# Kernel tuning notes

Hardware: AMD Instinct MI355X
Metric: run time of the kernel (lower is better)

## Reference

```python
import jax, jax.numpy as jnp
import numpy as np

EPS = 0.1
MAX_ITER = 100
THRESH = 0.1


def setup_inputs() -> dict:
    key = jax.random.key(0)
    k1, k2, k3, k4 = jax.random.split(key, 4)
    N, P1, P2, D = 4, 1024, 1024, 16
    x = jax.random.normal(k1, (N, P1, D), dtype=jnp.float32)
    y = jax.random.normal(k2, (N, P2, D), dtype=jnp.float32)
    wx = jax.random.uniform(k3, (N, P1), dtype=jnp.float32)
    wy = jax.random.uniform(k4, (N, P2), dtype=jnp.float32)
    # normalize to probability weights (typical usage for empirical measures)
    wx = wx / jnp.sum(wx, axis=-1, keepdims=True)
    wy = wy / jnp.sum(wy, axis=-1, keepdims=True)
    return {"x": x, "y": y, "wx": wx, "wy": wy}


def _cost_matrix(x, y):
    # |x_i - y_j|^1 summed over feature dim -> [N, P1, P2]
    return jnp.sum(jnp.abs(x[:, :, None, :] - y[:, None, :, :]), axis=-1)


def reference(x, y, wx, wy):
    C = _cost_matrix(x, y)                     # [N, P1, P2]
    mu, nu = wx, wy                            # [N, P1], [N, P2]
    log_mu = jnp.log(mu + 1e-8)
    log_nu = jnp.log(nu + 1e-8)

    def M(u, v):
        # (-C_ij + u_i + v_j) / eps
        return (-C + u[:, :, None] + v[:, None, :]) / EPS

    def step(carry, _):
        u, v, done = carry
        u_new = EPS * (log_mu - jax.nn.logsumexp(M(u, v), axis=-1)) + u
        v_new = EPS * (log_nu - jax.nn.logsumexp(M(u_new, v), axis=-2)) + v
        err = jnp.mean(jnp.sum(jnp.abs(u_new - u), axis=-1))
        # emulate torch's early break: freeze u,v once converged
        u_out = jnp.where(done, u, u_new)
        v_out = jnp.where(done, v, v_new)
        done = done | (err < THRESH)
        return (u_out, v_out, done), None

    u0 = jnp.zeros_like(mu)
    v0 = jnp.zeros_like(nu)
    (u, v, _), _ = jax.lax.scan(step, (u0, v0, jnp.array(False)), None, length=MAX_ITER)

    pi = jnp.exp(M(u, v))                      # transport plan [N, P1, P2]
    cost = jnp.sum(pi * C, axis=(-2, -1))      # [N]  (reduction='none')
    return cost, pi, C
```

## Files before the change

### kernel.cpp

```cpp
#include <hip/hip_runtime.h>

static constexpr int   NB      = 4;
static constexpr int   PP      = 1024;
static constexpr int   DD      = 16;
static constexpr float EPSV    = 0.1f;
static constexpr float KE      = 14.42695041f;
static constexpr float KL      = 0.0693147181f;
static constexpr int   MAXIT   = 100;
static constexpr float THRESHV = 0.1f;

static constexpr int NBLK = 256;
static constexpr int NTHR = 512;

__device__ __forceinline__ float fexp2(float v) { return __builtin_amdgcn_exp2f(v); }
__device__ __forceinline__ float flog2(float v) { return __builtin_amdgcn_logf(v); }

static constexpr size_t WS_BYTES = (4096 + 16) * 4;

static constexpr int VSNAP_OFF = 131072;
static constexpr int ERR_OFF   = 262144;

__device__ __forceinline__ float aload(const float* p) {
    return __hip_atomic_load(p, __ATOMIC_RELAXED, __HIP_MEMORY_SCOPE_AGENT);
}
__device__ __forceinline__ void astore(float* p, float v) {
    __hip_atomic_store(p, v, __ATOMIC_RELAXED, __HIP_MEMORY_SCOPE_AGENT);
}
__device__ __forceinline__ unsigned aloadu(const unsigned* p) {
    return __hip_atomic_load(p, __ATOMIC_RELAXED, __HIP_MEMORY_SCOPE_AGENT);
}
__device__ __forceinline__ void astoreu(unsigned* p, unsigned v) {
    __hip_atomic_store(p, v, __ATOMIC_RELAXED, __HIP_MEMORY_SCOPE_AGENT);
}
__device__ __forceinline__ float2 aload2(const float* p) {
    unsigned long long v = __hip_atomic_load((const unsigned long long*)p,
                                             __ATOMIC_RELAXED, __HIP_MEMORY_SCOPE_AGENT);
    union { unsigned long long u; float f[2]; } c; c.u = v;
    return make_float2(c.f[0], c.f[1]);
}
__device__ __forceinline__ void astore2(float* p, float a, float b) {
    union { unsigned long long u; float f[2]; } c; c.f[0] = a; c.f[1] = b;
    __hip_atomic_store((unsigned long long*)p, c.u,
                       __ATOMIC_RELAXED, __HIP_MEMORY_SCOPE_AGENT);
}

__device__ __forceinline__ void gbar_group(unsigned* ws32, int n, int g, unsigned gen) {
    __syncthreads();
    if (threadIdx.x < 64) {
        if (threadIdx.x == 0) astoreu(ws32 + (n * 64 + g) * 16, gen);
        const unsigned* sp = ws32 + (n * 64 + threadIdx.x) * 16;
        while (__ballot(aloadu(sp) >= gen) != ~0ull)
            __builtin_amdgcn_s_sleep(1);
    }
    __syncthreads();
}
__device__ __forceinline__ void gbar_all(unsigned* ws32, int b, unsigned gen) {
    __syncthreads();
    if (threadIdx.x < 64) {
        if (threadIdx.x == 0) astoreu(ws32 + b * 16, gen);
        for (;;) {
            bool ok = true;
            #pragma unroll
            for (int q = 0; q < 4; ++q)
                ok &= (aloadu(ws32 + (q * 64 + threadIdx.x) * 16) >= gen);
            if (__ballot(ok) == ~0ull) break;
            __builtin_amdgcn_s_sleep(1);
        }
    }
    __syncthreads();
}

__global__ __launch_bounds__(NTHR, 2)
void sinkhorn_kernel(const float* __restrict__ x, const float* __restrict__ y,
                     const float* __restrict__ wx, const float* __restrict__ wy,
                     float* __restrict__ out, float* __restrict__ ws)
{
    __shared__ float rt[16 * PP];
    __shared__ float sbuf[PP];
    __shared__ float cred[8];
    __shared__ int   Ts;

    unsigned* ws32 = (unsigned*)ws;
    unsigned* Tslot = ws32 + 4096;

    float* out_cost = out;
    float* out_pi   = out + NB;
    float* out_C    = out + NB + (size_t)NB * PP * PP;

    const int b   = blockIdx.x;
    const int n   = b >> 6;
    const int g   = b & 63;
    const int i0  = g * 16;
    const int w   = threadIdx.x >> 6;
    const int l   = threadIdx.x & 63;
    const int tid = threadIdx.x;

    float* sc  = out_C + (size_t)n * PP * PP;
    float* esc = sc + ERR_OFF;

    float4 xr[2][4];
    #pragma unroll
    for (int rr = 0; rr < 2; ++rr) {
        const float4* xp = (const float4*)(x + ((size_t)n * PP + (i0 + 2 * w + rr)) * DD);
        #pragma unroll
        for (int q = 0; q < 4; ++q) xr[rr][q] = xp[q];
    }
    #pragma unroll 4
    for (int k = 0; k < 16; ++k) {
        int j = l + 64 * k;
        const float4* yp = (const float4*)(y + ((size_t)n * PP + j) * DD);
        float4 y0 = yp[0], y1 = yp[1], y2 = yp[2], y3 = yp[3];
        #pragma unroll
        for (int rr = 0; rr < 2; ++rr) {
            float c = fabsf(xr[rr][0].x - y0.x) + fabsf(xr[rr][0].y - y0.y)
                    + fabsf(xr[rr][0].z - y0.z) + fabsf(xr[rr][0].w - y0.w)
                    + fabsf(xr[rr][1].x - y1.x) + fabsf(xr[rr][1].y - y1.y)
                    + fabsf(xr[rr][1].z - y1.z) + fabsf(xr[rr][1].w - y1.w)
                    + fabsf(xr[rr][2].x - y2.x) + fabsf(xr[rr][2].y - y2.y)
                    + fabsf(xr[rr][2].z - y2.z) + fabsf(xr[rr][2].w - y2.w)
                    + fabsf(xr[rr][3].x - y3.x) + fabsf(xr[rr][3].y - y3.y)
                    + fabsf(xr[rr][3].z - y3.z) + fabsf(xr[rr][3].w - y3.w);
            rt[(2 * w + rr) * PP + j] = c;
        }
    }

    float4 yc[2][4];
    #pragma unroll
    for (int c = 0; c < 2; ++c) {
        const float4* yp = (const float4*)(y + ((size_t)n * PP + (i0 + 2 * w + c)) * DD);
        #pragma unroll
        for (int q = 0; q < 4; ++q) yc[c][q] = yp[q];
    }
    float2 c2[16];
    #pragma unroll 4
    for (int k = 0; k < 16; ++k) {
        const float4* xp = (const float4*)(x + ((size_t)n * PP + (l + 64 * k)) * DD);
        float4 x0 = xp[0], x1 = xp[1], x2 = xp[2], x3 = xp[3];
        float cc[2];
        #pragma unroll
        for (int c = 0; c < 2; ++c) {
            cc[c] = fabsf(x0.x - yc[c][0].x) + fabsf(x0.y - yc[c][0].y)
                  + fabsf(x0.z - yc[c][0].z) + fabsf(x0.w - yc[c][0].w)
                  + fabsf(x1.x - yc[c][1].x) + fabsf(x1.y - yc[c][1].y)
                  + fabsf(x1.z - yc[c][1].z) + fabsf(x1.w - yc[c][1].w)
                  + fabsf(x2.x - yc[c][2].x) + fabsf(x2.y - yc[c][2].y)
                  + fabsf(x2.z - yc[c][2].z) + fabsf(x2.w - yc[c][2].w)
                  + fabsf(x3.x - yc[c][3].x) + fabsf(x3.y - yc[c][3].y)
                  + fabsf(x3.z - yc[c][3].z) + fabsf(x3.w - yc[c][3].w);
        }
        c2[k] = make_float2(cc[0], cc[1]);
    }

    float u_loc[2], lmu[2], lnu[2];
    #pragma unroll
    for (int rr = 0; rr < 2; ++rr) {
        u_loc[rr] = 0.f;
        lmu[rr] = __logf(wx[n * PP + i0 + 2 * w + rr] + 1e-8f);
        lnu[rr] = __logf(wy[n * PP + i0 + 2 * w + rr] + 1e-8f);
    }

    #pragma unroll 1
    for (int t = 0; t < MAXIT; ++t) {
        if (t == 0) {
            sbuf[2 * tid] = 0.f; sbuf[2 * tid + 1] = 0.f;
        } else {
            float2 vp = aload2(sc + VSNAP_OFF + (size_t)(t - 1) * PP + 2 * tid);
            sbuf[2 * tid] = vp.x; sbuf[2 * tid + 1] = vp.y;
        }
        __syncthreads();

        float unew[2], werr;
        {
            float4 tt[2][4];
            float m0 = -3.4e38f, m1 = -3.4e38f;
            #pragma unroll
            for (int k = 0; k < 4; ++k) {
                int j = 256 * k + 4 * l;
                float4 v4 = *(const float4*)&sbuf[j];
                float4 ca = *(const float4*)&rt[(2 * w) * PP + j];
                float4 cb = *(const float4*)&rt[(2 * w + 1) * PP + j];
                tt[0][k] = make_float4(v4.x - ca.x, v4.y - ca.y, v4.z - ca.z, v4.w - ca.w);
                tt[1][k] = make_float4(v4.x - cb.x, v4.y - cb.y, v4.z - cb.z, v4.w - cb.w);
                m0 = fmaxf(m0, fmaxf(fmaxf(tt[0][k].x, tt[0][k].y), fmaxf(tt[0][k].z, tt[0][k].w)));
                m1 = fmaxf(m1, fmaxf(fmaxf(tt[1][k].x, tt[1][k].y), fmaxf(tt[1][k].z, tt[1][k].w)));
            }
            #pragma unroll
            for (int off = 32; off >= 1; off >>= 1) {
                m0 = fmaxf(m0, __shfl_xor(m0, off));
                m1 = fmaxf(m1, __shfl_xor(m1, off));
            }
            float s0 = 0.f, s1 = 0.f;
            #pragma unroll
            for (int k = 0; k < 4; ++k) {
                s0 += fexp2((tt[0][k].x - m0) * KE) + fexp2((tt[0][k].y - m0) * KE)
                    + fexp2((tt[0][k].z - m0) * KE) + fexp2((tt[0][k].w - m0) * KE);
                s1 += fexp2((tt[1][k].x - m1) * KE) + fexp2((tt[1][k].y - m1) * KE)
                    + fexp2((tt[1][k].z - m1) * KE) + fexp2((tt[1][k].w - m1) * KE);
            }
            #pragma unroll
            for (int off = 32; off >= 1; off >>= 1) {
                s0 += __shfl_xor(s0, off);
                s1 += __shfl_xor(s1, off);
            }
            unew[0] = EPSV * lmu[0] - (m0 + KL * flog2(s0));
            unew[1] = EPSV * lmu[1] - (m1 + KL * flog2(s1));
            werr = fabsf(unew[0] - u_loc[0]) + fabsf(unew[1] - u_loc[1]);
            u_loc[0] = unew[0]; u_loc[1] = unew[1];
            if (l == 0) {
                astore2(sc + (size_t)t * PP + i0 + 2 * w, unew[0], unew[1]);
                cred[w] = werr;
            }
        }

        __syncthreads();
        if (tid < 64) {
            if (tid == 0) {
                float es = cred[0] + cred[1] + cred[2] + cred[3]
                         + cred[4] + cred[5] + cred[6] + cred[7];
                astore(esc + t * 64 + g, es);
                astoreu(ws32 + (n * 64 + g) * 16, (unsigned)(2 * t + 1));
            }
            const unsigned* sp = ws32 + (n * 64 + tid) * 16;
            while (__ballot(aloadu(sp) >= (unsigned)(2 * t + 1)) != ~0ull)
                __builtin_amdgcn_s_sleep(1);
        }
        __syncthreads();

        {
            float2 up = aload2(sc + (size_t)t * PP + 2 * tid);
            sbuf[2 * tid] = up.x; sbuf[2 * tid + 1] = up.y;
        }
        __syncthreads();

        float vnew[2];
        {
            float tt0[16], tt1[16], m0 = -3.4e38f, m1 = -3.4e38f;
            #pragma unroll
            for (int k = 0; k < 16; ++k) {
                float uu = sbuf[l + 64 * k];
                tt0[k] = uu - c2[k].x;
                tt1[k] = uu - c2[k].y;
                m0 = fmaxf(m0, tt0[k]);
                m1 = fmaxf(m1, tt1[k]);
            }
            #pragma unroll
            for (int off = 32; off >= 1; off >>= 1) {
                m0 = fmaxf(m0, __shfl_xor(m0, off));
                m1 = fmaxf(m1, __shfl_xor(m1, off));
            }
            float s0 = 0.f, s1 = 0.f;
            #pragma unroll
            for (int k = 0; k < 16; ++k) {
                s0 += fexp2((tt0[k] - m0) * KE);
                s1 += fexp2((tt1[k] - m1) * KE);
            }
            #pragma unroll
            for (int off = 32; off >= 1; off >>= 1) {
                s0 += __shfl_xor(s0, off);
                s1 += __shfl_xor(s1, off);
            }
            vnew[0] = EPSV * lnu[0] - (m0 + KL * flog2(s0));
            vnew[1] = EPSV * lnu[1] - (m1 + KL * flog2(s1));
            if (l == 0)
                astore2(sc + VSNAP_OFF + (size_t)t * PP + i0 + 2 * w, vnew[0], vnew[1]);
        }

        gbar_group(ws32, n, g, (unsigned)(2 * t + 2));
    }

    gbar_all(ws32, b, (unsigned)(2 * MAXIT + 1));

    if (b == 0 && tid < 64) {
        float s1 = 0.f;
        #pragma unroll 1
        for (int q = 0; q < NB; ++q) {
            const float* ebase = out_C + (size_t)q * PP * PP + ERR_OFF + l * 64;
            #pragma unroll
            for (int k = 0; k < 32; ++k) { float2 e2 = aload2(ebase + 2 * k); s1 += e2.x + e2.y; }
        }
        unsigned long long b1 = __ballot(s1 < THRESHV * (float)NB);
        float s2 = 1e30f;
        if (64 + l < MAXIT) {
            s2 = 0.f;
            #pragma unroll 1
            for (int q = 0; q < NB; ++q) {
                const float* ebase = out_C + (size_t)q * PP * PP + ERR_OFF + (64 + l) * 64;
                #pragma unroll
                for (int k = 0; k < 32; ++k) { float2 e2 = aload2(ebase + 2 * k); s2 += e2.x + e2.y; }
            }
        }
        unsigned long long b2 = __ballot(s2 < THRESHV * (float)NB);
        int T = b1 ? (__ffsll((long long)b1) - 1)
                   : (b2 ? 64 + (__ffsll((long long)b2) - 1) : MAXIT - 1);
        if (tid == 0) astoreu(Tslot, (unsigned)(T + 1));
    }
    if (tid == 0) {
        unsigned tv;
        while ((tv = aloadu(Tslot)) == 0u) __builtin_amdgcn_s_sleep(4);
        Ts = (int)tv - 1;
    }
    __syncthreads();
    const int T = Ts;

    {
        float2 up = aload2(sc + (size_t)T * PP + i0 + 2 * w);
        u_loc[0] = up.x; u_loc[1] = up.y;
        float2 vp = aload2(sc + VSNAP_OFF + (size_t)T * PP + 2 * tid);
        sbuf[2 * tid] = vp.x; sbuf[2 * tid + 1] = vp.y;
    }
    gbar_group(ws32, n, g, (unsigned)(2 * MAXIT + 2));

    float cacc = 0.f;
    #pragma unroll
    for (int rr = 0; rr < 2; ++rr) {
        int r = 2 * w + rr;
        int i = i0 + r;
        float un = u_loc[rr];
        #pragma unroll
        for (int k = 0; k < 4; ++k) {
            int j = 256 * k + 4 * l;
            float4 c4 = *(const float4*)&rt[r * PP + j];
            float4 v4 = *(const float4*)&sbuf[j];
            float4 p4;
            p4.x = fexp2((un + v4.x - c4.x) * KE);
            p4.y = fexp2((un + v4.y - c4.y) * KE);
            p4.z = fexp2((un + v4.z - c4.z) * KE);
            p4.w = fexp2((un + v4.w - c4.w) * KE);
            *(float4*)&out_pi[((size_t)n * PP + i) * PP + j] = p4;
            *(float4*)&out_C [((size_t)n * PP + i) * PP + j] = c4;
            cacc += p4.x * c4.x + p4.y * c4.y + p4.z * c4.z + p4.w * c4.w;
        }
    }
    #pragma unroll
    for (int off = 32; off >= 1; off >>= 1) cacc += __shfl_xor(cacc, off);
    if (l == 0) cred[w] = cacc;
    __syncthreads();
    if (tid == 0) {
        float s = 0.f;
        #pragma unroll
        for (int q = 0; q < 8; ++q) s += cred[q];
        atomicAdd(&out_cost[n], s);
    }
}

extern "C" void kernel_launch(void* const* d_in, const int* in_sizes, int n_in,
                              void* d_out, int out_size, void* d_ws, size_t ws_size,
                              hipStream_t stream) {
    const float* x  = (const float*)d_in[0];
    const float* y  = (const float*)d_in[1];
    const float* wx = (const float*)d_in[2];
    const float* wy = (const float*)d_in[3];
    float* out = (float*)d_out;
    float* ws  = (float*)d_ws;

    (void)hipMemsetAsync(d_ws, 0, WS_BYTES, stream);
    (void)hipMemsetAsync(d_out, 0, NB * sizeof(float), stream);

    hipLaunchKernelGGL(sinkhorn_kernel, dim3(NBLK), dim3(NTHR), 0, stream,
                       x, y, wx, wy, out, ws);
}
```

Measured before the change: 792.5 us.

## Add early exit from Sinkhorn loop once convergence detected across batches

Moves the per-iteration error computation to after the u barrier, so every block derives the error from the gathered u, and has group 0 publish per-iteration error sums to workspace. Group 0 checks whether any iteration has met the global threshold and sets a per-batch exit flag, which lets blocks stop iterating shortly after convergence instead of always running all 100 iterations. The end-of-loop all-block barrier becomes a DONE marker wait in block 0. The error buffer is pre-filled with large values via an extra memset. This adds a flag load per iteration and more cross-block coordination.

```diff
diff --git a/kernel.cpp b/kernel.cpp
--- a/kernel.cpp
+++ b/kernel.cpp
@@ -11,14 +11,16 @@
 
 static constexpr int NBLK = 256;
 static constexpr int NTHR = 512;
+static constexpr unsigned DONEG = 1000000u;
 
 __device__ __forceinline__ float fexp2(float v) { return __builtin_amdgcn_exp2f(v); }
 __device__ __forceinline__ float flog2(float v) { return __builtin_amdgcn_logf(v); }
 
-static constexpr size_t WS_BYTES = (4096 + 16) * 4;
+static constexpr int    ERR_F_OFF     = 4352;
+static constexpr size_t WS_ZERO_BYTES = 4352 * 4;
+static constexpr size_t ERR_BYTES    = 512 * 4;
 
 static constexpr int VSNAP_OFF = 131072;
-static constexpr int ERR_OFF   = 262144;
 
 __device__ __forceinline__ float aload(const float* p) {
     return __hip_atomic_load(p, __ATOMIC_RELAXED, __HIP_MEMORY_SCOPE_AGENT);
@@ -51,21 +53,6 @@
         const unsigned* sp = ws32 + (n * 64 + threadIdx.x) * 16;
         while (__ballot(aloadu(sp) >= gen) != ~0ull)
             __builtin_amdgcn_s_sleep(1);
-    }
-    __syncthreads();
-}
-__device__ __forceinline__ void gbar_all(unsigned* ws32, int b, unsigned gen) {
-    __syncthreads();
-    if (threadIdx.x < 64) {
-        if (threadIdx.x == 0) astoreu(ws32 + b * 16, gen);
-        for (;;) {
-            bool ok = true;
-            #pragma unroll
-            for (int q = 0; q < 4; ++q)
-                ok &= (aloadu(ws32 + (q * 64 + threadIdx.x) * 16) >= gen);
-            if (__ballot(ok) == ~0ull) break;
-            __builtin_amdgcn_s_sleep(1);
-        }
     }
     __syncthreads();
 }
@@ -80,8 +67,10 @@
     __shared__ float cred[8];
     __shared__ int   Ts;
 
-    unsigned* ws32 = (unsigned*)ws;
+    unsigned* ws32  = (unsigned*)ws;
     unsigned* Tslot = ws32 + 4096;
+    unsigned* exitf = ws32 + 4104;
+    float*    ews   = ws + ERR_F_OFF;
 
     float* out_cost = out;
     float* out_pi   = out + NB;
@@ -95,8 +84,7 @@
     const int l   = threadIdx.x & 63;
     const int tid = threadIdx.x;
 
-    float* sc  = out_C + (size_t)n * PP * PP;
-    float* esc = sc + ERR_OFF;
+    float* sc = out_C + (size_t)n * PP * PP;
 
     float4 xr[2][4];
     #pragma unroll
@@ -151,16 +139,22 @@
         c2[k] = make_float2(cc[0], cc[1]);
     }
 
-    float u_loc[2], lmu[2], lnu[2];
+    float lmu[2], lnu[2];
     #pragma unroll
     for (int rr = 0; rr < 2; ++rr) {
-        u_loc[rr] = 0.f;
         lmu[rr] = __logf(wx[n * PP + i0 + 2 * w + rr] + 1e-8f);
         lnu[rr] = __logf(wy[n * PP + i0 + 2 * w + rr] + 1e-8f);
     }
 
+    float uprev0 = 0.f, uprev1 = 0.f;
+
     #pragma unroll 1
     for (int t = 0; t < MAXIT; ++t) {
+        if (t >= 2) {
+            unsigned ef = aloadu(exitf + n);
+            if (ef != 0u && t >= (int)ef + 1) break;
+        }
+
         if (t == 0) {
             sbuf[2 * tid] = 0.f; sbuf[2 * tid + 1] = 0.f;
         } else {
@@ -169,7 +163,6 @@
         }
         __syncthreads();
 
-        float unew[2], werr;
         {
             float4 tt[2][4];
             float m0 = -3.4e38f, m1 = -3.4e38f;
@@ -202,37 +195,24 @@
                 s0 += __shfl_xor(s0, off);
                 s1 += __shfl_xor(s1, off);
             }
-            unew[0] = EPSV * lmu[0] - (m0 + KL * flog2(s0));
-            unew[1] = EPSV * lmu[1] - (m1 + KL * flog2(s1));
-            werr = fabsf(unew[0] - u_loc[0]) + fabsf(unew[1] - u_loc[1]);
-            u_loc[0] = unew[0]; u_loc[1] = unew[1];
-            if (l == 0) {
-                astore2(sc + (size_t)t * PP + i0 + 2 * w, unew[0], unew[1]);
-                cred[w] = werr;
-            }
-        }
-
-        __syncthreads();
-        if (tid < 64) {
-            if (tid == 0) {
-                float es = cred[0] + cred[1] + cred[2] + cred[3]
-                         + cred[4] + cred[5] + cred[6] + cred[7];
-                astore(esc + t * 64 + g, es);
-                astoreu(ws32 + (n * 64 + g) * 16, (unsigned)(2 * t + 1));
-            }
-            const unsigned* sp = ws32 + (n * 64 + tid) * 16;
-            while (__ballot(aloadu(sp) >= (unsigned)(2 * t + 1)) != ~0ull)
-                __builtin_amdgcn_s_sleep(1);
-        }
-        __syncthreads();
+            float un0 = EPSV * lmu[0] - (m0 + KL * flog2(s0));
+            float un1 = EPSV * lmu[1] - (m1 + KL * flog2(s1));
+            if (l == 0) astore2(sc + (size_t)t * PP + i0 + 2 * w, un0, un1);
+        }
+
+        gbar_group(ws32, n, g, (unsigned)(2 * t + 1));
 
         {
             float2 up = aload2(sc + (size_t)t * PP + 2 * tid);
             sbuf[2 * tid] = up.x; sbuf[2 * tid + 1] = up.y;
+            float we = fabsf(up.x - uprev0) + fabsf(up.y - uprev1);
+            uprev0 = up.x; uprev1 = up.y;
+            #pragma unroll
+            for (int off = 32; off >= 1; off >>= 1) we += __shfl_xor(we, off);
+            if (l == 0) cred[w] = we;
         }
         __syncthreads();
 
-        float vnew[2];
         {
             float tt0[16], tt1[16], m0 = -3.4e38f, m1 = -3.4e38f;
             #pragma unroll
@@ -259,56 +239,71 @@
                 s0 += __shfl_xor(s0, off);
                 s1 += __shfl_xor(s1, off);
             }
-            vnew[0] = EPSV * lnu[0] - (m0 + KL * flog2(s0));
-            vnew[1] = EPSV * lnu[1] - (m1 + KL * flog2(s1));
+            float vn0 = EPSV * lnu[0] - (m0 + KL * flog2(s0));
+            float vn1 = EPSV * lnu[1] - (m1 + KL * flog2(s1));
             if (l == 0)
-                astore2(sc + VSNAP_OFF + (size_t)t * PP + i0 + 2 * w, vnew[0], vnew[1]);
-        }
-
-        gbar_group(ws32, n, g, (unsigned)(2 * t + 2));
-    }
-
-    gbar_all(ws32, b, (unsigned)(2 * MAXIT + 1));
+                astore2(sc + VSNAP_OFF + (size_t)t * PP + i0 + 2 * w, vn0, vn1);
+        }
+        if (g == 0 && tid == 0) {
+            float es = cred[0] + cred[1] + cred[2] + cred[3]
+                     + cred[4] + cred[5] + cred[6] + cred[7];
+            astore(ews + n * 128 + t, es);
+        }
+
+        __syncthreads();
+        if (tid < 64) {
+            if (tid == 0) astoreu(ws32 + (n * 64 + g) * 16, (unsigned)(2 * t + 2));
+            if (g == 0) {
+                float s1f = aload(ews + 0 * 128 + tid) + aload(ews + 1 * 128 + tid)
+                          + aload(ews + 2 * 128 + tid) + aload(ews + 3 * 128 + tid);
+                float s2f = aload(ews + 0 * 128 + 64 + tid) + aload(ews + 1 * 128 + 64 + tid)
+                          + aload(ews + 2 * 128 + 64 + tid) + aload(ews + 3 * 128 + 64 + tid);
+                unsigned long long bb = __ballot(s1f < THRESHV * (float)NB)
+                                      | __ballot(s2f < THRESHV * (float)NB);
+                if (bb != 0ull && tid == 0 && aloadu(exitf + n) == 0u)
+                    astoreu(exitf + n, (unsigned)(t + 1));
+            }
+            const unsigned* sp = ws32 + (n * 64 + tid) * 16;
+            while (__ballot(aloadu(sp) >= (unsigned)(2 * t + 2)) != ~0ull)
+                __builtin_amdgcn_s_sleep(1);
+        }
+        __syncthreads();
+    }
+
+    if (g == 0 && tid == 0) astoreu(ws32 + (n * 64) * 16, DONEG);
 
     if (b == 0 && tid < 64) {
-        float s1 = 0.f;
-        #pragma unroll 1
-        for (int q = 0; q < NB; ++q) {
-            const float* ebase = out_C + (size_t)q * PP * PP + ERR_OFF + l * 64;
-            #pragma unroll
-            for (int k = 0; k < 32; ++k) { float2 e2 = aload2(ebase + 2 * k); s1 += e2.x + e2.y; }
-        }
-        unsigned long long b1 = __ballot(s1 < THRESHV * (float)NB);
-        float s2 = 1e30f;
-        if (64 + l < MAXIT) {
-            s2 = 0.f;
-            #pragma unroll 1
-            for (int q = 0; q < NB; ++q) {
-                const float* ebase = out_C + (size_t)q * PP * PP + ERR_OFF + (64 + l) * 64;
-                #pragma unroll
-                for (int k = 0; k < 32; ++k) { float2 e2 = aload2(ebase + 2 * k); s2 += e2.x + e2.y; }
-            }
-        }
-        unsigned long long b2 = __ballot(s2 < THRESHV * (float)NB);
+        for (;;) {
+            bool ok = (tid >= 4) || (aloadu(ws32 + tid * 64 * 16) >= DONEG);
+            if (__ballot(ok) == ~0ull) break;
+            __builtin_amdgcn_s_sleep(2);
+        }
+        float s1f = aload(ews + 0 * 128 + tid) + aload(ews + 1 * 128 + tid)
+                  + aload(ews + 2 * 128 + tid) + aload(ews + 3 * 128 + tid);
+        float s2f = aload(ews + 0 * 128 + 64 + tid) + aload(ews + 1 * 128 + 64 + tid)
+                  + aload(ews + 2 * 128 + 64 + tid) + aload(ews + 3 * 128 + 64 + tid);
+        unsigned long long b1 = __ballot(s1f < THRESHV * (float)NB);
+        unsigned long long b2 = __ballot(s2f < THRESHV * (float)NB);
         int T = b1 ? (__ffsll((long long)b1) - 1)
                    : (b2 ? 64 + (__ffsll((long long)b2) - 1) : MAXIT - 1);
         if (tid == 0) astoreu(Tslot, (unsigned)(T + 1));
     }
     if (tid == 0) {
         unsigned tv;
-        while ((tv = aloadu(Tslot)) == 0u) __builtin_amdgcn_s_sleep(4);
+        while ((tv = aloadu(Tslot)) == 0u) __builtin_amdgcn_s_sleep(2);
         Ts = (int)tv - 1;
     }
     __syncthreads();
     const int T = Ts;
 
+    float u_loc[2];
     {
         float2 up = aload2(sc + (size_t)T * PP + i0 + 2 * w);
         u_loc[0] = up.x; u_loc[1] = up.y;
         float2 vp = aload2(sc + VSNAP_OFF + (size_t)T * PP + 2 * tid);
         sbuf[2 * tid] = vp.x; sbuf[2 * tid + 1] = vp.y;
     }
-    gbar_group(ws32, n, g, (unsigned)(2 * MAXIT + 2));
+    gbar_group(ws32, n, g, DONEG + 1u);
 
     float cacc = 0.f;
     #pragma unroll
@@ -353,7 +348,8 @@
     float* out = (float*)d_out;
     float* ws  = (float*)d_ws;
 
-    (void)hipMemsetAsync(d_ws, 0, WS_BYTES, stream);
+    (void)hipMemsetAsync(d_ws, 0, WS_ZERO_BYTES, stream);
+    (void)hipMemsetAsync((char*)d_ws + WS_ZERO_BYTES, 0x7f, ERR_BYTES, stream);
     (void)hipMemsetAsync(d_out, 0, NB * sizeof(float), stream);
 
     hipLaunchKernelGGL(sinkhorn_kernel, dim3(NBLK), dim3(NTHR), 0, stream,
```

After: 787.3 us. No clear change (-0.7%).
